# Optimization experiments

Hardware: AMD Instinct MI355X
Metric: run time of the kernel (lower is better)

The kernel has to match this reference:

```python
import jax, jax.numpy as jnp
import numpy as np

PAD = 0
TOP_K = 2
NEG_INF = -1e30  # stand-in for -inf that stays finite under fp16/bf16


def setup_inputs() -> dict:
    key = jax.random.key(0)
    ks = jax.random.split(key, 8)
    B, T, L = 128, 16, 64
    V, D, F, E = 50000, 512, 256, 8
    sample = jax.random.randint(ks[0], (B, T, L), 0, V, dtype=jnp.int32)
    emb_table = jax.random.normal(ks[1], (V, D), dtype=jnp.float32) * (1.0 / np.sqrt(D))
    expert_q = jax.random.normal(ks[2], (E, D), dtype=jnp.float32) * (1.0 / np.sqrt(D))
    expert_Wk = jax.random.normal(ks[3], (E, D, D), dtype=jnp.float32) * (1.0 / np.sqrt(D))
    gate_W = jax.random.normal(ks[4], (E, D), dtype=jnp.float32) * (1.0 / np.sqrt(D))
    gate_b = jax.random.normal(ks[5], (E,), dtype=jnp.float32) * 0.01
    trans_W = jax.random.normal(ks[6], (F, D), dtype=jnp.float32) * (1.0 / np.sqrt(D))
    trans_b = jax.random.normal(ks[7], (F,), dtype=jnp.float32) * 0.01
    return {"sample": sample, "emb_table": emb_table, "expert_q": expert_q,
            "expert_Wk": expert_Wk, "gate_W": gate_W, "gate_b": gate_b,
            "trans_W": trans_W, "trans_b": trans_b}


def _forward(sample, emb_table, expert_q, expert_Wk, gate_W, gate_b, trans_W, trans_b):
    L = sample.shape[-1]
    flat = sample.reshape(-1, L)                      # (N, L)
    N = flat.shape[0]
    token_emb = emb_table[flat]                        # (N, L, D) gather
    seqs_mask = flat == PAD                            # (N, L) True at pad
    token_emb = jnp.where(seqs_mask[:, :, None], 0.0, token_emb)
    seqs_len = jnp.sum(~seqs_mask, axis=1, keepdims=True)  # (N, 1)

    # --- MoE pooling over experts ---
    # scores_e = (x @ Wk_e^T) . q_e == x @ (Wk_e^T q_e); fold linearly.
    proj = jnp.einsum('eod,eo->ed', expert_Wk, expert_q)      # (E, D)
    scores = jnp.einsum('nld,ed->nle', token_emb, proj)       # (N, L, E)
    scores = jnp.where(seqs_mask[:, :, None], NEG_INF, scores)
    all_pad = jnp.all(seqs_mask, axis=1)                      # (N,)
    scores = jnp.where(all_pad[:, None, None], 1.0, scores)
    attn = jax.nn.softmax(scores, axis=1)                     # (N, L, E)
    expert_out = jnp.einsum('nle,nld->ned', attn, token_emb)  # (N, E, D)

    # gating: mean over tokens (zeros included, matching torch .mean(dim=1))
    gate_in = jnp.mean(token_emb, axis=1)                     # (N, D)
    gate_scores = gate_in @ gate_W.T + gate_b                 # (N, E)
    topv, topi = jax.lax.top_k(gate_scores, TOP_K)            # (N, K)
    gate_w = jax.nn.softmax(topv, axis=-1)                    # (N, K)
    full_w = jnp.zeros_like(gate_scores).at[jnp.arange(N)[:, None], topi].set(gate_w)
    pooled = jnp.einsum('ne,ned->nd', full_w, expert_out)     # (N, D)

    pooled = jnp.where(seqs_len == 0, 0.0, pooled)
    text_emb = pooled.reshape(*sample.shape[:-1], -1)         # (B, T, D)
    out = jax.nn.gelu(text_emb @ trans_W.T + trans_b, approximate=False)
    return out                                                # (B, T, F)


def reference(sample, emb_table, expert_q, expert_Wk, gate_W, gate_b, trans_W, trans_b):
    return _forward(sample, emb_table, expert_q, expert_Wk, gate_W, gate_b, trans_W, trans_b)
```

## Files before the change

kernel.cpp:

```cpp
#include <hip/hip_runtime.h>
#include <math.h>

#define L 64
#define D 512
#define E 8
#define F 256
#define NEG_INF -1e30f

__global__ void projA_kernel(const float* __restrict__ Wk, const float* __restrict__ q,
                             float* __restrict__ part) {
    const int e = blockIdx.x >> 3, oc = blockIdx.x & 7;
    const int d = threadIdx.x;
    const float* wb = Wk + ((size_t)e * D + oc * 64) * D + d;
    const float* qb = q + e * D + oc * 64;
    float acc = 0.f;
    #pragma unroll 8
    for (int o = 0; o < 64; ++o) acc += wb[(size_t)o * D] * qb[o];
    part[(size_t)blockIdx.x * D + d] = acc;
}

__global__ void projB_kernel(const float* __restrict__ part, float* __restrict__ proj) {
    const int i = blockIdx.x * blockDim.x + threadIdx.x;
    const int e = i >> 9, d = i & (D - 1);
    float s = 0.f;
    #pragma unroll
    for (int oc = 0; oc < 8; ++oc) s += part[(size_t)(e * 8 + oc) * D + d];
    proj[i] = s;
}

__global__ void transp_kernel(const float* __restrict__ W, float* __restrict__ wT) {
    const int d = blockIdx.x, f = threadIdx.x;
    wT[(size_t)d * F + f] = W[(size_t)f * D + d];
}

__launch_bounds__(512, 4)
__global__ void row_kernel(const int* __restrict__ sample,
                           const float* __restrict__ emb_table,
                           const float* __restrict__ proj,
                           const float* __restrict__ gate_W,
                           const float* __restrict__ gate_b,
                           float* __restrict__ pooled) {
    __shared__ float red[8][D];
    __shared__ int   idx_s[L];
    __shared__ float msk[L];
    __shared__ float scr[2][L];
    __shared__ float att2[2][L];
    __shared__ float cf[L];
    __shared__ float gred[64];
    __shared__ float gsc[E];
    __shared__ float wsel[2];
    __shared__ int   esel[2];
    __shared__ int   allpad;

    const int n    = blockIdx.x;
    const int tid  = threadIdx.x;
    const int lane = tid & 63;
    const int wv   = tid >> 6;

    if (tid < L) {
        int ix = sample[n * L + tid];
        idx_s[tid] = ix;
        msk[tid] = (ix != 0) ? 1.f : 0.f;
    }
    __syncthreads();

    float4 a0[8], a1[8];
    #pragma unroll
    for (int j = 0; j < 8; ++j) {
        const float4* src = (const float4*)(emb_table + (size_t)idx_s[wv * 8 + j] * D);
        a0[j] = src[lane];
        a1[j] = src[lane + 64];
    }

    {
        float4 s0 = {0.f, 0.f, 0.f, 0.f}, s1 = {0.f, 0.f, 0.f, 0.f};
        #pragma unroll
        for (int j = 0; j < 8; ++j) {
            float m = msk[wv * 8 + j];
            s0.x += m * a0[j].x; s0.y += m * a0[j].y; s0.z += m * a0[j].z; s0.w += m * a0[j].w;
            s1.x += m * a1[j].x; s1.y += m * a1[j].y; s1.z += m * a1[j].z; s1.w += m * a1[j].w;
        }
        ((float4*)red[wv])[lane]      = s0;
        ((float4*)red[wv])[lane + 64] = s1;
    }
    __syncthreads();

    float g = 0.f;
    #pragma unroll
    for (int w = 0; w < 8; ++w) g += red[w][tid];
    const float gi = g * (1.f / 64.f);

    {
        float p[E];
        #pragma unroll
        for (int e = 0; e < E; ++e) p[e] = gi * gate_W[e * D + tid];
        #pragma unroll
        for (int e = 0; e < E; ++e) {
            float v = p[e];
            #pragma unroll
            for (int off = 32; off; off >>= 1) v += __shfl_xor(v, off, 64);
            if (lane == 0) gred[wv * E + e] = v;
        }
    }
    __syncthreads();
    if (tid < E) {
        float s = gate_b[tid];
        #pragma unroll
        for (int w = 0; w < 8; ++w) s += gred[w * E + tid];
        gsc[tid] = s;
    }
    __syncthreads();

    if (tid == 0) {
        int b0 = 0; float v0 = gsc[0];
        for (int e = 1; e < E; ++e) if (gsc[e] > v0) { v0 = gsc[e]; b0 = e; }
        int b1 = -1; float v1 = -3.4e38f;
        for (int e = 0; e < E; ++e) if (e != b0 && gsc[e] > v1) { v1 = gsc[e]; b1 = e; }
        float ex  = expf(v1 - v0);
        float inv = 1.f / (1.f + ex);
        wsel[0] = inv; wsel[1] = ex * inv;
        esel[0] = b0;  esel[1] = b1;
        float cnt = 0.f;
        for (int l = 0; l < L; ++l) cnt += msk[l];
        allpad = (cnt == 0.f) ? 1 : 0;
    }
    __syncthreads();

    {
        const float4* pe0 = (const float4*)(proj + esel[0] * D);
        const float4* pe1 = (const float4*)(proj + esel[1] * D);
        float4 b00 = pe0[lane], b01 = pe0[lane + 64];
        float4 b10 = pe1[lane], b11 = pe1[lane + 64];
        #pragma unroll
        for (int j = 0; j < 8; ++j) {
            float s0 = a0[j].x*b00.x + a0[j].y*b00.y + a0[j].z*b00.z + a0[j].w*b00.w
                     + a1[j].x*b01.x + a1[j].y*b01.y + a1[j].z*b01.z + a1[j].w*b01.w;
            float s1 = a0[j].x*b10.x + a0[j].y*b10.y + a0[j].z*b10.z + a0[j].w*b10.w
                     + a1[j].x*b11.x + a1[j].y*b11.y + a1[j].z*b11.z + a1[j].w*b11.w;
            #pragma unroll
            for (int off = 32; off; off >>= 1) {
                s0 += __shfl_xor(s0, off, 64);
                s1 += __shfl_xor(s1, off, 64);
            }
            if (lane == 0) {
                int l = wv * 8 + j;
                bool real = (msk[l] != 0.f);
                scr[0][l] = real ? s0 : NEG_INF;
                scr[1][l] = real ? s1 : NEG_INF;
            }
        }
    }
    __syncthreads();

    if (tid < 128) {
        int k = wv;
        float s = scr[k][lane];
        float m = s;
        #pragma unroll
        for (int off = 32; off; off >>= 1) m = fmaxf(m, __shfl_xor(m, off, 64));
        float pex = expf(s - m);
        float sum = pex;
        #pragma unroll
        for (int off = 32; off; off >>= 1) sum += __shfl_xor(sum, off, 64);
        att2[k][lane] = pex / sum;
    }
    __syncthreads();
    if (tid < L) cf[tid] = wsel[0] * att2[0][tid] + wsel[1] * att2[1][tid];
    __syncthreads();

    {
        float4 s0 = {0.f, 0.f, 0.f, 0.f}, s1 = {0.f, 0.f, 0.f, 0.f};
        #pragma unroll
        for (int j = 0; j < 8; ++j) {
            float c = cf[wv * 8 + j];
            s0.x += c * a0[j].x; s0.y += c * a0[j].y; s0.z += c * a0[j].z; s0.w += c * a0[j].w;
            s1.x += c * a1[j].x; s1.y += c * a1[j].y; s1.z += c * a1[j].z; s1.w += c * a1[j].w;
        }
        ((float4*)red[wv])[lane]      = s0;
        ((float4*)red[wv])[lane + 64] = s1;
    }
    __syncthreads();

    float acc = 0.f;
    #pragma unroll
    for (int w = 0; w < 8; ++w) acc += red[w][tid];
    if (allpad) acc = 0.f;
    pooled[(size_t)n * D + tid] = acc;
}

__launch_bounds__(256, 4)
__global__ void out_kernel(const float* __restrict__ pooled,
                           const float* __restrict__ wT,
                           const float* __restrict__ trans_b,
                           float* __restrict__ out) {
    __shared__ float pl[8 * D];
    const int tid  = threadIdx.x;
    const int lane = tid & 63;
    const int w    = tid >> 6;
    const int n0   = blockIdx.x * 8;

    {
        const float4* src = (const float4*)(pooled + (size_t)n0 * D);
        float4* dst = (float4*)pl;
        #pragma unroll
        for (int i = 0; i < 4; ++i) dst[tid + 256 * i] = src[tid + 256 * i];
    }
    __syncthreads();

    const float* pl0 = pl + (2 * w) * D;
    const float* pl1 = pl0 + D;
    const float4* wT4 = (const float4*)wT;
    float4 acc0 = {0.f,0.f,0.f,0.f}, acc1 = {0.f,0.f,0.f,0.f};
    #pragma unroll 4
    for (int d = 0; d < D; ++d) {
        float4 wt = wT4[d * 64 + lane];
        float p0 = pl0[d], p1 = pl1[d];
        acc0.x += p0*wt.x; acc0.y += p0*wt.y; acc0.z += p0*wt.z; acc0.w += p0*wt.w;
        acc1.x += p1*wt.x; acc1.y += p1*wt.y; acc1.z += p1*wt.z; acc1.w += p1*wt.w;
    }

    float4 b4 = ((const float4*)trans_b)[lane];
    float4 o0, o1;
    #define GELU(v) (0.5f * (v) * (1.f + erff((v) * 0.70710678118654752f)))
    o0.x = GELU(acc0.x + b4.x); o0.y = GELU(acc0.y + b4.y);
    o0.z = GELU(acc0.z + b4.z); o0.w = GELU(acc0.w + b4.w);
    o1.x = GELU(acc1.x + b4.x); o1.y = GELU(acc1.y + b4.y);
    o1.z = GELU(acc1.z + b4.z); o1.w = GELU(acc1.w + b4.w);
    #undef GELU
    ((float4*)(out + (size_t)(n0 + 2 * w) * F))[lane]     = o0;
    ((float4*)(out + (size_t)(n0 + 2 * w + 1) * F))[lane] = o1;
}

extern "C" void kernel_launch(void* const* d_in, const int* in_sizes, int n_in,
                              void* d_out, int out_size, void* d_ws, size_t ws_size,
                              hipStream_t stream) {
    const int*   sample    = (const int*)d_in[0];
    const float* emb_table = (const float*)d_in[1];
    const float* expert_q  = (const float*)d_in[2];
    const float* expert_Wk = (const float*)d_in[3];
    const float* gate_W    = (const float*)d_in[4];
    const float* gate_b    = (const float*)d_in[5];
    const float* trans_W   = (const float*)d_in[6];
    const float* trans_b   = (const float*)d_in[7];
    float* out = (float*)d_out;

    const int N = in_sizes[0] / L;

    float* proj   = (float*)d_ws;
    float* pooled = proj + E * D;
    float* part   = pooled + (size_t)N * D;
    float* wT     = part + E * 8 * D;
    (void)ws_size; (void)n_in; (void)out_size;

    projA_kernel<<<E * 8, D, 0, stream>>>(expert_Wk, expert_q, part);
    projB_kernel<<<(E * D) / 256, 256, 0, stream>>>(part, proj);
    transp_kernel<<<D, F, 0, stream>>>(trans_W, wT);
    row_kernel<<<N, 512, 0, stream>>>(sample, emb_table, proj, gate_W, gate_b, pooled);
    out_kernel<<<N / 8, 256, 0, stream>>>(pooled, wT, trans_b, out);
}
```

Before: 112.9 us.

## Software-pipeline embedding gathers across rows and merge prep kernels

Each row_kernel block now handles 8 rows and double-buffers register tiles, so the next row's embedding gather is issued while the current row is reduced. It also uses a custom barrier macro and moves the mask count into the gate reduction. projA is split into more, smaller blocks, projB and the transpose are fused into one prep kernel, and out_kernel computes 4 rows per wave with vectorised shared loads. The costs are much higher register pressure (launch bounds 2 blocks), only 256 row blocks in flight, and a barrier that relies on inline asm.

```diff
diff --git a/kernel.cpp b/kernel.cpp
--- a/kernel.cpp
+++ b/kernel.cpp
@@ -6,34 +6,162 @@
 #define E 8
 #define F 256
 #define NEG_INF -1e30f
+#define RPB 8
+
+#define BAR() do { asm volatile("s_waitcnt lgkmcnt(0)" ::: "memory"); \
+                   __builtin_amdgcn_s_barrier();                      \
+                   asm volatile("" ::: "memory"); } while (0)
 
 __global__ void projA_kernel(const float* __restrict__ Wk, const float* __restrict__ q,
                              float* __restrict__ part) {
-    const int e = blockIdx.x >> 3, oc = blockIdx.x & 7;
+    const int e = blockIdx.x >> 5, oc = blockIdx.x & 31;
     const int d = threadIdx.x;
-    const float* wb = Wk + ((size_t)e * D + oc * 64) * D + d;
-    const float* qb = q + e * D + oc * 64;
+    const float* wb = Wk + ((size_t)e * D + oc * 16) * D + d;
+    const float* qb = q + e * D + oc * 16;
     float acc = 0.f;
-    #pragma unroll 8
-    for (int o = 0; o < 64; ++o) acc += wb[(size_t)o * D] * qb[o];
+    #pragma unroll
+    for (int o = 0; o < 16; ++o) acc += wb[(size_t)o * D] * qb[o];
     part[(size_t)blockIdx.x * D + d] = acc;
 }
 
-__global__ void projB_kernel(const float* __restrict__ part, float* __restrict__ proj) {
-    const int i = blockIdx.x * blockDim.x + threadIdx.x;
-    const int e = i >> 9, d = i & (D - 1);
-    float s = 0.f;
-    #pragma unroll
-    for (int oc = 0; oc < 8; ++oc) s += part[(size_t)(e * 8 + oc) * D + d];
-    proj[i] = s;
-}
-
-__global__ void transp_kernel(const float* __restrict__ W, float* __restrict__ wT) {
-    const int d = blockIdx.x, f = threadIdx.x;
-    wT[(size_t)d * F + f] = W[(size_t)f * D + d];
-}
-
-__launch_bounds__(512, 4)
+__global__ void prep2_kernel(const float* __restrict__ part, const float* __restrict__ W,
+                             float* __restrict__ proj, float* __restrict__ wT) {
+    const int b = blockIdx.x;
+    if (b < 8) {
+        const int i = b * 512 + threadIdx.x;
+        const int e = i >> 9, d = i & (D - 1);
+        float s = 0.f;
+        #pragma unroll
+        for (int oc = 0; oc < 32; ++oc) s += part[(size_t)(e * 32 + oc) * D + d];
+        proj[i] = s;
+    } else {
+        const int i = (b - 8) * 512 + threadIdx.x;
+        const int f = i & (F - 1), d = i >> 8;
+        wT[(size_t)d * F + f] = W[(size_t)f * D + d];
+    }
+}
+
+#define BODY(C0, C1, MC, N0, N1, MN, ROW, PRE)                                      \
+  {                                                                                 \
+    if (PRE) {                                                                      \
+      const int* sp = sample + ((ROW) + 1) * L + wv * 8;                            \
+      _Pragma("unroll")                                                             \
+      for (int j = 0; j < 8; ++j) {                                                 \
+        int ix = sp[j];                                                             \
+        MN[j] = (ix != 0) ? 1.f : 0.f;                                              \
+        const float4* src = (const float4*)(emb_table + (size_t)ix * D);            \
+        N0[j] = src[lane]; N1[j] = src[lane + 64];                                  \
+      }                                                                             \
+    }                                                                               \
+    {                                    \
+      float4 s0 = {0,0,0,0}, s1 = {0,0,0,0};                                        \
+      _Pragma("unroll")                                                             \
+      for (int j = 0; j < 8; ++j) {                                                 \
+        float m = MC[j];                                                            \
+        s0.x += m*C0[j].x; s0.y += m*C0[j].y; s0.z += m*C0[j].z; s0.w += m*C0[j].w; \
+        s1.x += m*C1[j].x; s1.y += m*C1[j].y; s1.z += m*C1[j].z; s1.w += m*C1[j].w; \
+      }                                                                             \
+      ((float4*)red[wv])[lane] = s0; ((float4*)red[wv])[lane + 64] = s1;            \
+    }                                                                               \
+    BAR();                                                                          \
+    {                                          \
+      float g = 0.f;                                                                \
+      _Pragma("unroll")                                                             \
+      for (int w = 0; w < 8; ++w) g += red[w][tid];                                 \
+      g *= (1.f / 64.f);                                                            \
+      _Pragma("unroll")                                                             \
+      for (int e = 0; e < E; ++e) {                                                 \
+        float v = g * gate_W[e * D + tid];                                          \
+        _Pragma("unroll")                                                           \
+        for (int off = 32; off; off >>= 1) v += __shfl_xor(v, off, 64);             \
+        if (lane == 0) gred[wv][e] = v;                                             \
+      }                                                                             \
+      if (lane == 0) {                                                              \
+        float c = 0.f;                                                              \
+        _Pragma("unroll")                                                           \
+        for (int j = 0; j < 8; ++j) c += MC[j];                                     \
+        gred[wv][E] = c;                                                            \
+      }                                                                             \
+    }                                                                               \
+    BAR();                                                                          \
+    if (tid == 0) {              \
+      float gs[E]; float cnt = 0.f;                                                 \
+      _Pragma("unroll")                                                             \
+      for (int e = 0; e < E; ++e) {                                                 \
+        float s = gate_b[e];                                                        \
+        _Pragma("unroll")                                                           \
+        for (int w = 0; w < 8; ++w) s += gred[w][e];                                \
+        gs[e] = s;                                                                  \
+      }                                                                             \
+      _Pragma("unroll")                                                             \
+      for (int w = 0; w < 8; ++w) cnt += gred[w][E];                                \
+      int b0 = 0; float v0 = gs[0];                                                 \
+      for (int e = 1; e < E; ++e) if (gs[e] > v0) { v0 = gs[e]; b0 = e; }           \
+      int b1 = -1; float v1 = -3.4e38f;                                             \
+      for (int e = 0; e < E; ++e) if (e != b0 && gs[e] > v1) { v1 = gs[e]; b1 = e; }\
+      float ex = expf(v1 - v0); float inv = 1.f / (1.f + ex);                       \
+      wsel[0] = inv; wsel[1] = ex * inv;                                            \
+      esel[0] = b0; esel[1] = b1;                                                   \
+      allpad = (cnt == 0.f) ? 1 : 0;                                                \
+    }                                                                               \
+    BAR();                                                                          \
+    {                               \
+      const float4* pe0 = (const float4*)(proj + esel[0] * D);                      \
+      const float4* pe1 = (const float4*)(proj + esel[1] * D);                      \
+      float4 b00 = pe0[lane], b01 = pe0[lane + 64];                                 \
+      float4 b10 = pe1[lane], b11 = pe1[lane + 64];                                 \
+      _Pragma("unroll")                                                             \
+      for (int j = 0; j < 8; ++j) {                                                 \
+        float s0 = C0[j].x*b00.x + C0[j].y*b00.y + C0[j].z*b00.z + C0[j].w*b00.w    \
+                 + C1[j].x*b01.x + C1[j].y*b01.y + C1[j].z*b01.z + C1[j].w*b01.w;   \
+        float s1 = C0[j].x*b10.x + C0[j].y*b10.y + C0[j].z*b10.z + C0[j].w*b10.w    \
+                 + C1[j].x*b11.x + C1[j].y*b11.y + C1[j].z*b11.z + C1[j].w*b11.w;   \
+        _Pragma("unroll")                                                           \
+        for (int off = 32; off; off >>= 1) {                                        \
+          s0 += __shfl_xor(s0, off, 64); s1 += __shfl_xor(s1, off, 64);             \
+        }                                                                           \
+        if (lane == 0) {                                                            \
+          scr[0][wv * 8 + j] = (MC[j] != 0.f) ? s0 : NEG_INF;                       \
+          scr[1][wv * 8 + j] = (MC[j] != 0.f) ? s1 : NEG_INF;                       \
+        }                                                                           \
+      }                                                                             \
+    }                                                                               \
+    BAR();                                                                          \
+    if (tid < 128) {                   \
+      float s = scr[wv][lane];                                                      \
+      float m = s;                                                                  \
+      _Pragma("unroll")                                                             \
+      for (int off = 32; off; off >>= 1) m = fmaxf(m, __shfl_xor(m, off, 64));      \
+      float pex = expf(s - m);                                                      \
+      float su = pex;                                                               \
+      _Pragma("unroll")                                                             \
+      for (int off = 32; off; off >>= 1) su += __shfl_xor(su, off, 64);             \
+      att2[wv][lane] = pex / su;                                                    \
+    }                                                                               \
+    BAR();                                                                          \
+    {         \
+      float w0 = wsel[0], w1 = wsel[1];                                             \
+      float4 s0 = {0,0,0,0}, s1 = {0,0,0,0};                                        \
+      _Pragma("unroll")                                                             \
+      for (int j = 0; j < 8; ++j) {                                                 \
+        float c = w0 * att2[0][wv * 8 + j] + w1 * att2[1][wv * 8 + j];              \
+        s0.x += c*C0[j].x; s0.y += c*C0[j].y; s0.z += c*C0[j].z; s0.w += c*C0[j].w; \
+        s1.x += c*C1[j].x; s1.y += c*C1[j].y; s1.z += c*C1[j].z; s1.w += c*C1[j].w; \
+      }                                                                             \
+      ((float4*)red[wv])[lane] = s0; ((float4*)red[wv])[lane + 64] = s1;            \
+    }                                                                               \
+    BAR();                                                                          \
+    {                                                                               \
+      float acc = 0.f;                                                              \
+      _Pragma("unroll")                                                             \
+      for (int w = 0; w < 8; ++w) acc += red[w][tid];                               \
+      if (allpad) acc = 0.f;                                                        \
+      pooled[(size_t)(ROW) * D + tid] = acc;                                        \
+    }                                                                               \
+    BAR();                                                                          \
+  }
+
+__launch_bounds__(512, 2)
 __global__ void row_kernel(const int* __restrict__ sample,
                            const float* __restrict__ emb_table,
                            const float* __restrict__ proj,
@@ -41,151 +169,37 @@
                            const float* __restrict__ gate_b,
                            float* __restrict__ pooled) {
     __shared__ float red[8][D];
-    __shared__ int   idx_s[L];
-    __shared__ float msk[L];
+    __shared__ float gred[8][E + 2];
     __shared__ float scr[2][L];
     __shared__ float att2[2][L];
-    __shared__ float cf[L];
-    __shared__ float gred[64];
-    __shared__ float gsc[E];
     __shared__ float wsel[2];
     __shared__ int   esel[2];
     __shared__ int   allpad;
 
-    const int n    = blockIdx.x;
     const int tid  = threadIdx.x;
     const int lane = tid & 63;
     const int wv   = tid >> 6;
-
-    if (tid < L) {
-        int ix = sample[n * L + tid];
-        idx_s[tid] = ix;
-        msk[tid] = (ix != 0) ? 1.f : 0.f;
-    }
-    __syncthreads();
-
-    float4 a0[8], a1[8];
-    #pragma unroll
-    for (int j = 0; j < 8; ++j) {
-        const float4* src = (const float4*)(emb_table + (size_t)idx_s[wv * 8 + j] * D);
-        a0[j] = src[lane];
-        a1[j] = src[lane + 64];
-    }
+    const int base = blockIdx.x * RPB;
+
+    float4 A0[8], A1[8], B0[8], B1[8];
+    float  ma[8], mb[8];
 
     {
-        float4 s0 = {0.f, 0.f, 0.f, 0.f}, s1 = {0.f, 0.f, 0.f, 0.f};
+        const int* sp = sample + base * L + wv * 8;
         #pragma unroll
         for (int j = 0; j < 8; ++j) {
-            float m = msk[wv * 8 + j];
-            s0.x += m * a0[j].x; s0.y += m * a0[j].y; s0.z += m * a0[j].z; s0.w += m * a0[j].w;
-            s1.x += m * a1[j].x; s1.y += m * a1[j].y; s1.z += m * a1[j].z; s1.w += m * a1[j].w;
+            int ix = sp[j];
+            ma[j] = (ix != 0) ? 1.f : 0.f;
+            const float4* src = (const float4*)(emb_table + (size_t)ix * D);
+            A0[j] = src[lane]; A1[j] = src[lane + 64];
         }
-        ((float4*)red[wv])[lane]      = s0;
-        ((float4*)red[wv])[lane + 64] = s1;
-    }
-    __syncthreads();
-
-    float g = 0.f;
-    #pragma unroll
-    for (int w = 0; w < 8; ++w) g += red[w][tid];
-    const float gi = g * (1.f / 64.f);
-
-    {
-        float p[E];
-        #pragma unroll
-        for (int e = 0; e < E; ++e) p[e] = gi * gate_W[e * D + tid];
-        #pragma unroll
-        for (int e = 0; e < E; ++e) {
-            float v = p[e];
-            #pragma unroll
-            for (int off = 32; off; off >>= 1) v += __shfl_xor(v, off, 64);
-            if (lane == 0) gred[wv * E + e] = v;
-        }
-    }
-    __syncthreads();
-    if (tid < E) {
-        float s = gate_b[tid];
-        #pragma unroll
-        for (int w = 0; w < 8; ++w) s += gred[w * E + tid];
-        gsc[tid] = s;
-    }
-    __syncthreads();
-
-    if (tid == 0) {
-        int b0 = 0; float v0 = gsc[0];
-        for (int e = 1; e < E; ++e) if (gsc[e] > v0) { v0 = gsc[e]; b0 = e; }
-        int b1 = -1; float v1 = -3.4e38f;
-        for (int e = 0; e < E; ++e) if (e != b0 && gsc[e] > v1) { v1 = gsc[e]; b1 = e; }
-        float ex  = expf(v1 - v0);
-        float inv = 1.f / (1.f + ex);
-        wsel[0] = inv; wsel[1] = ex * inv;
-        esel[0] = b0;  esel[1] = b1;
-        float cnt = 0.f;
-        for (int l = 0; l < L; ++l) cnt += msk[l];
-        allpad = (cnt == 0.f) ? 1 : 0;
-    }
-    __syncthreads();
-
-    {
-        const float4* pe0 = (const float4*)(proj + esel[0] * D);
-        const float4* pe1 = (const float4*)(proj + esel[1] * D);
-        float4 b00 = pe0[lane], b01 = pe0[lane + 64];
-        float4 b10 = pe1[lane], b11 = pe1[lane + 64];
-        #pragma unroll
-        for (int j = 0; j < 8; ++j) {
-            float s0 = a0[j].x*b00.x + a0[j].y*b00.y + a0[j].z*b00.z + a0[j].w*b00.w
-                     + a1[j].x*b01.x + a1[j].y*b01.y + a1[j].z*b01.z + a1[j].w*b01.w;
-            float s1 = a0[j].x*b10.x + a0[j].y*b10.y + a0[j].z*b10.z + a0[j].w*b10.w
-                     + a1[j].x*b11.x + a1[j].y*b11.y + a1[j].z*b11.z + a1[j].w*b11.w;
-            #pragma unroll
-            for (int off = 32; off; off >>= 1) {
-                s0 += __shfl_xor(s0, off, 64);
-                s1 += __shfl_xor(s1, off, 64);
-            }
-            if (lane == 0) {
-                int l = wv * 8 + j;
-                bool real = (msk[l] != 0.f);
-                scr[0][l] = real ? s0 : NEG_INF;
-                scr[1][l] = real ? s1 : NEG_INF;
-            }
-        }
-    }
-    __syncthreads();
-
-    if (tid < 128) {
-        int k = wv;
-        float s = scr[k][lane];
-        float m = s;
-        #pragma unroll
-        for (int off = 32; off; off >>= 1) m = fmaxf(m, __shfl_xor(m, off, 64));
-        float pex = expf(s - m);
-        float sum = pex;
-        #pragma unroll
-        for (int off = 32; off; off >>= 1) sum += __shfl_xor(sum, off, 64);
-        att2[k][lane] = pex / sum;
-    }
-    __syncthreads();
-    if (tid < L) cf[tid] = wsel[0] * att2[0][tid] + wsel[1] * att2[1][tid];
-    __syncthreads();
-
-    {
-        float4 s0 = {0.f, 0.f, 0.f, 0.f}, s1 = {0.f, 0.f, 0.f, 0.f};
-        #pragma unroll
-        for (int j = 0; j < 8; ++j) {
-            float c = cf[wv * 8 + j];
-            s0.x += c * a0[j].x; s0.y += c * a0[j].y; s0.z += c * a0[j].z; s0.w += c * a0[j].w;
-            s1.x += c * a1[j].x; s1.y += c * a1[j].y; s1.z += c * a1[j].z; s1.w += c * a1[j].w;
-        }
-        ((float4*)red[wv])[lane]      = s0;
-        ((float4*)red[wv])[lane + 64] = s1;
-    }
-    __syncthreads();
-
-    float acc = 0.f;
-    #pragma unroll
-    for (int w = 0; w < 8; ++w) acc += red[w][tid];
-    if (allpad) acc = 0.f;
-    pooled[(size_t)n * D + tid] = acc;
+    }
+
+    #pragma unroll 1
+    for (int i = 0; i < RPB; i += 2) {
+        BODY(A0, A1, ma, B0, B1, mb, base + i,     (i + 1 < RPB));
+        BODY(B0, B1, mb, A0, A1, ma, base + i + 1, (i + 2 < RPB));
+    }
 }
 
 __launch_bounds__(256, 4)
@@ -193,42 +207,53 @@
                            const float* __restrict__ wT,
                            const float* __restrict__ trans_b,
                            float* __restrict__ out) {
-    __shared__ float pl[8 * D];
-    const int tid  = threadIdx.x;
-    const int lane = tid & 63;
-    const int w    = tid >> 6;
-    const int n0   = blockIdx.x * 8;
+    __shared__ float pl[16 * D];
+    const int tid = threadIdx.x, lane = tid & 63, w = tid >> 6;
+    const int n0 = blockIdx.x * 16;
 
     {
         const float4* src = (const float4*)(pooled + (size_t)n0 * D);
         float4* dst = (float4*)pl;
         #pragma unroll
-        for (int i = 0; i < 4; ++i) dst[tid + 256 * i] = src[tid + 256 * i];
+        for (int i = 0; i < 8; ++i) dst[tid + 256 * i] = src[tid + 256 * i];
     }
     __syncthreads();
 
-    const float* pl0 = pl + (2 * w) * D;
-    const float* pl1 = pl0 + D;
+    const float* p0 = pl + (w * 4) * D;
     const float4* wT4 = (const float4*)wT;
-    float4 acc0 = {0.f,0.f,0.f,0.f}, acc1 = {0.f,0.f,0.f,0.f};
-    #pragma unroll 4
-    for (int d = 0; d < D; ++d) {
-        float4 wt = wT4[d * 64 + lane];
-        float p0 = pl0[d], p1 = pl1[d];
-        acc0.x += p0*wt.x; acc0.y += p0*wt.y; acc0.z += p0*wt.z; acc0.w += p0*wt.w;
-        acc1.x += p1*wt.x; acc1.y += p1*wt.y; acc1.z += p1*wt.z; acc1.w += p1*wt.w;
+    float4 a0 = {0,0,0,0}, a1 = {0,0,0,0}, a2 = {0,0,0,0}, a3 = {0,0,0,0};
+    #pragma unroll 8
+    for (int d4 = 0; d4 < D / 4; ++d4) {
+        float4 q0 = *(const float4*)&p0[d4 * 4];
+        float4 q1 = *(const float4*)&p0[D + d4 * 4];
+        float4 q2 = *(const float4*)&p0[2 * D + d4 * 4];
+        float4 q3 = *(const float4*)&p0[3 * D + d4 * 4];
+        #pragma unroll
+        for (int t = 0; t < 4; ++t) {
+            float4 wt = wT4[(d4 * 4 + t) * 64 + lane];
+            float e0 = (t == 0) ? q0.x : (t == 1) ? q0.y : (t == 2) ? q0.z : q0.w;
+            float e1 = (t == 0) ? q1.x : (t == 1) ? q1.y : (t == 2) ? q1.z : q1.w;
+            float e2 = (t == 0) ? q2.x : (t == 1) ? q2.y : (t == 2) ? q2.z : q2.w;
+            float e3 = (t == 0) ? q3.x : (t == 1) ? q3.y : (t == 2) ? q3.z : q3.w;
+            a0.x += e0*wt.x; a0.y += e0*wt.y; a0.z += e0*wt.z; a0.w += e0*wt.w;
+            a1.x += e1*wt.x; a1.y += e1*wt.y; a1.z += e1*wt.z; a1.w += e1*wt.w;
+            a2.x += e2*wt.x; a2.y += e2*wt.y; a2.z += e2*wt.z; a2.w += e2*wt.w;
+            a3.x += e3*wt.x; a3.y += e3*wt.y; a3.z += e3*wt.z; a3.w += e3*wt.w;
+        }
     }
 
     float4 b4 = ((const float4*)trans_b)[lane];
-    float4 o0, o1;
     #define GELU(v) (0.5f * (v) * (1.f + erff((v) * 0.70710678118654752f)))
-    o0.x = GELU(acc0.x + b4.x); o0.y = GELU(acc0.y + b4.y);
-    o0.z = GELU(acc0.z + b4.z); o0.w = GELU(acc0.w + b4.w);
-    o1.x = GELU(acc1.x + b4.x); o1.y = GELU(acc1.y + b4.y);
-    o1.z = GELU(acc1.z + b4.z); o1.w = GELU(acc1.w + b4.w);
+    float4 o;
+    o.x = GELU(a0.x + b4.x); o.y = GELU(a0.y + b4.y); o.z = GELU(a0.z + b4.z); o.w = GELU(a0.w + b4.w);
+    ((float4*)(out + (size_t)(n0 + w * 4 + 0) * F))[lane] = o;
+    o.x = GELU(a1.x + b4.x); o.y = GELU(a1.y + b4.y); o.z = GELU(a1.z + b4.z); o.w = GELU(a1.w + b4.w);
+    ((float4*)(out + (size_t)(n0 + w * 4 + 1) * F))[lane] = o;
+    o.x = GELU(a2.x + b4.x); o.y = GELU(a2.y + b4.y); o.z = GELU(a2.z + b4.z); o.w = GELU(a2.w + b4.w);
+    ((float4*)(out + (size_t)(n0 + w * 4 + 2) * F))[lane] = o;
+    o.x = GELU(a3.x + b4.x); o.y = GELU(a3.y + b4.y); o.z = GELU(a3.z + b4.z); o.w = GELU(a3.w + b4.w);
+    ((float4*)(out + (size_t)(n0 + w * 4 + 3) * F))[lane] = o;
     #undef GELU
-    ((float4*)(out + (size_t)(n0 + 2 * w) * F))[lane]     = o0;
-    ((float4*)(out + (size_t)(n0 + 2 * w + 1) * F))[lane] = o1;
 }
 
 extern "C" void kernel_launch(void* const* d_in, const int* in_sizes, int n_in,
@@ -249,12 +274,11 @@
     float* proj   = (float*)d_ws;
     float* pooled = proj + E * D;
     float* part   = pooled + (size_t)N * D;
-    float* wT     = part + E * 8 * D;
+    float* wT     = part + E * 32 * D;
     (void)ws_size; (void)n_in; (void)out_size;
 
-    projA_kernel<<<E * 8, D, 0, stream>>>(expert_Wk, expert_q, part);
-    projB_kernel<<<(E * D) / 256, 256, 0, stream>>>(part, proj);
-    transp_kernel<<<D, F, 0, stream>>>(trans_W, wT);
-    row_kernel<<<N, 512, 0, stream>>>(sample, emb_table, proj, gate_W, gate_b, pooled);
-    out_kernel<<<N / 8, 256, 0, stream>>>(pooled, wT, trans_b, out);
-}
+    projA_kernel<<<E * 32, D, 0, stream>>>(expert_Wk, expert_q, part);
+    prep2_kernel<<<8 + (D * F) / 512, 512, 0, stream>>>(part, trans_W, proj, wT);
+    row_kernel<<<N / RPB, 512, 0, stream>>>(sample, emb_table, proj, gate_W, gate_b, pooled);
+    out_kernel<<<N / 16, 256, 0, stream>>>(pooled, wT, trans_b, out);
+}
```

Result: slower. 162.3 us (+43.7%).
